# Kernel optimization log

Measured on AMD Instinct MI355X. Metric: run time of the kernel, lower is better.

Reference implementation:

```python
import jax, jax.numpy as jnp
import numpy as np

D_MODEL = 2048
NUM_HEADS = 16
HEAD_DIM = D_MODEL // NUM_HEADS
EPS = 1e-6


def setup_inputs() -> dict:
    key = jax.random.key(0)
    ks = jax.random.split(key, 5)
    B, S = 1, 4096
    scale = 1.0 / np.sqrt(D_MODEL)
    return {
        "x": jax.random.normal(ks[0], (B, S, D_MODEL), dtype=jnp.float32),
        "wq": jax.random.normal(ks[1], (D_MODEL, D_MODEL), dtype=jnp.float32) * scale,
        "wk": jax.random.normal(ks[2], (D_MODEL, D_MODEL), dtype=jnp.float32) * scale,
        "wv": jax.random.normal(ks[3], (D_MODEL, D_MODEL), dtype=jnp.float32) * scale,
        "wo": jax.random.normal(ks[4], (D_MODEL, D_MODEL), dtype=jnp.float32) * scale,
        "q_norm_w": jnp.ones((HEAD_DIM,), dtype=jnp.float32),
        "k_norm_w": jnp.ones((HEAD_DIM,), dtype=jnp.float32),
    }


def _rmsnorm(x, w):
    rms = jnp.sqrt(jnp.mean(x * x, axis=-1, keepdims=True) + EPS)
    return x / rms * w


def reference(x, wq, wk, wv, wo, q_norm_w, k_norm_w):
    B, S, _ = x.shape
    # nn.Linear: y = x @ W.T ; split heads -> [B, H, S, Dh]
    def proj(w):
        return (x @ w.T).reshape(B, S, NUM_HEADS, HEAD_DIM).transpose(0, 2, 1, 3)
    q = _rmsnorm(proj(wq), q_norm_w)
    k = _rmsnorm(proj(wk), k_norm_w)
    v = proj(wv)
    scale = 1.0 / np.sqrt(HEAD_DIM)
    attn = jnp.einsum("bhqd,bhkd->bhqk", q, k) * scale  # [B,H,S,S]
    attn = jax.nn.softmax(attn, axis=-1)
    out = jnp.einsum("bhqk,bhkd->bhqd", attn, v)
    out = out.transpose(0, 2, 1, 3).reshape(B, S, D_MODEL)
    return out @ wo.T
```

## Files before the change

kernel.cpp:

```cpp
#include <hip/hip_runtime.h>
#include <hip/hip_bf16.h>

#define S 4096
#define D 2048
#define NH 16
#define HD 128

typedef __attribute__((ext_vector_type(8))) short bf16x8;
typedef __attribute__((ext_vector_type(4))) float f32x4;

typedef __attribute__((address_space(1))) char glob_char;
typedef __attribute__((address_space(3))) char lds_char_t;

__device__ __forceinline__ void gld16(const void* g, void* l) {
    __builtin_amdgcn_global_load_lds((const glob_char*)g, (lds_char_t*)l, 16, 0, 0);
}

__device__ __forceinline__ unsigned short f2b(float f) {
    union { float f; unsigned u; } c; c.f = f;
    unsigned r = c.u + 0x7fff + ((c.u >> 16) & 1);
    return (unsigned short)(r >> 16);
}

__device__ __forceinline__ float fexp2(float x) {
#if __has_builtin(__builtin_amdgcn_exp2f)
    return __builtin_amdgcn_exp2f(x);
#else
    return __expf(x * 0.6931471805599453f);
#endif
}

__global__ __launch_bounds__(256) void cvt_all(
    const float* __restrict__ x,  const float* __restrict__ wq,
    const float* __restrict__ wk, const float* __restrict__ wv,
    const float* __restrict__ wo,
    unsigned short* __restrict__ xb, unsigned short* __restrict__ wqkvb,
    unsigned short* __restrict__ wob)
{
    const int z = blockIdx.y;
    const float* src; unsigned short* dst; int n4;
    if (z == 0)      { src = x;  dst = xb;                        n4 = (S * D) / 4; }
    else if (z == 1) { src = wq; dst = wqkvb;                     n4 = (D * D) / 4; }
    else if (z == 2) { src = wk; dst = wqkvb + (size_t)D * D;     n4 = (D * D) / 4; }
    else if (z == 3) { src = wv; dst = wqkvb + 2 * (size_t)D * D; n4 = (D * D) / 4; }
    else             { src = wo; dst = wob;                       n4 = (D * D) / 4; }
    int i = blockIdx.x * 256 + threadIdx.x;
    if (i < n4) {
        float4 v = ((const float4*)src)[i];
        ushort4 o;
        o.x = f2b(v.x); o.y = f2b(v.y); o.z = f2b(v.z); o.w = f2b(v.w);
        ((ushort4*)dst)[i] = o;
    }
}

template<int OUTMODE>
__global__ __launch_bounds__(256) void gemm_nt(
    const unsigned short* __restrict__ A, const unsigned short* __restrict__ B,
    void* __restrict__ O0, void* __restrict__ O1, void* __restrict__ O2,
    const float* __restrict__ qw, const float* __restrict__ kw)
{
    __shared__ short As[128 * 32];
    __shared__ short Bs[128 * 32];
    __shared__ float red[2][128];

    const int tid = threadIdx.x;
    const int m0 = blockIdx.y * 128, n0 = blockIdx.x * 128;
    const int w = tid >> 6, lane = tid & 63, col = lane & 15, quad = lane >> 4;
    const int mw = (w >> 1) * 64, nw = (w & 1) * 64;

    const int r0 = tid >> 2, k80 = (tid & 3) << 3;
    const size_t aoff = (size_t)(m0 + r0) * 2048 + k80;
    const size_t boff = (size_t)(n0 + r0) * 2048 + k80;

    f32x4 acc[4][4];
    #pragma unroll
    for (int i = 0; i < 4; ++i)
        #pragma unroll
        for (int j = 0; j < 4; ++j)
            #pragma unroll
            for (int r = 0; r < 4; ++r) acc[i][j][r] = 0.0f;

    for (int k0 = 0; k0 < 2048; k0 += 32) {
        gld16(&A[aoff + k0],               &As[tid * 8]);
        gld16(&A[aoff + 64 * 2048 + k0],   &As[(tid + 256) * 8]);
        gld16(&B[boff + k0],               &Bs[tid * 8]);
        gld16(&B[boff + 64 * 2048 + k0],   &Bs[(tid + 256) * 8]);
        __syncthreads();
        bf16x8 af[4], bf[4];
        #pragma unroll
        for (int i = 0; i < 4; ++i)
            af[i] = *(const bf16x8*)&As[(mw + 16 * i + col) * 32 + quad * 8];
        #pragma unroll
        for (int j = 0; j < 4; ++j)
            bf[j] = *(const bf16x8*)&Bs[(nw + 16 * j + col) * 32 + quad * 8];
        #pragma unroll
        for (int i = 0; i < 4; ++i)
            #pragma unroll
            for (int j = 0; j < 4; ++j)
                acc[i][j] = __builtin_amdgcn_mfma_f32_16x16x32_bf16(af[i], bf[j], acc[i][j], 0, 0, 0);
        __syncthreads();
    }

    if (OUTMODE == 1) {
        float* C = (float*)O0;
        #pragma unroll
        for (int i = 0; i < 4; ++i)
            #pragma unroll
            for (int j = 0; j < 4; ++j)
                #pragma unroll
                for (int r = 0; r < 4; ++r)
                    C[(size_t)(m0 + mw + 16 * i + quad * 4 + r) * 2048 + n0 + nw + 16 * j + col] = acc[i][j][r];
    } else {
        const int sel = n0 >> 11;
        if (sel == 2) {
            unsigned short* VtO = (unsigned short*)O2;
            #pragma unroll
            for (int i = 0; i < 4; ++i)
                #pragma unroll
                for (int j = 0; j < 4; ++j) {
                    int n = (n0 & 2047) + nw + 16 * j + col;
                    int hh = n >> 7, dv = n & 127;
                    ushort4 pk;
                    pk.x = f2b(acc[i][j][0]); pk.y = f2b(acc[i][j][1]);
                    pk.z = f2b(acc[i][j][2]); pk.w = f2b(acc[i][j][3]);
                    *(ushort4*)&VtO[(size_t)hh * (HD * S) + (size_t)dv * S +
                                    m0 + mw + 16 * i + quad * 4] = pk;
                }
        } else {
            unsigned short* C = (unsigned short*)(sel == 0 ? O0 : O1);
            const int nc0 = (n0 & 2047) + nw + col;
            const float* wgt = (sel == 0) ? qw : kw;
            const float extra = (sel == 0)
                ? 0.08838834764831845f * 1.4426950408889634f : 1.0f;
            float wv[4];
            #pragma unroll
            for (int j = 0; j < 4; ++j) wv[j] = wgt[nw + 16 * j + col];
            float rsc[4][4];
            #pragma unroll
            for (int i = 0; i < 4; ++i)
                #pragma unroll
                for (int r = 0; r < 4; ++r) {
                    float ss = 0.0f;
                    #pragma unroll
                    for (int j = 0; j < 4; ++j) ss += acc[i][j][r] * acc[i][j][r];
                    #pragma unroll
                    for (int d = 1; d < 16; d <<= 1) ss += __shfl_xor(ss, d, 64);
                    if (col == 0) red[w & 1][mw + 16 * i + quad * 4 + r] = ss;
                }
            __syncthreads();
            #pragma unroll
            for (int i = 0; i < 4; ++i)
                #pragma unroll
                for (int r = 0; r < 4; ++r) {
                    float tot = red[0][mw + 16 * i + quad * 4 + r] + red[1][mw + 16 * i + quad * 4 + r];
                    rsc[i][r] = rsqrtf(tot * (1.0f / HD) + 1e-6f) * extra;
                }
            #pragma unroll
            for (int i = 0; i < 4; ++i)
                #pragma unroll
                for (int j = 0; j < 4; ++j)
                    #pragma unroll
                    for (int r = 0; r < 4; ++r)
                        C[(size_t)(m0 + mw + 16 * i + quad * 4 + r) * 2048 + nc0 + 16 * j] =
                            f2b(acc[i][j][r] * rsc[i][r] * wv[j]);
        }
    }
}

struct FlashSmem {
    short Ks[2][8192];
    short Vs[2][8192];
    short Ps[8192];
};

__global__ __launch_bounds__(256, 2) void flash_mfma(
    const unsigned short* __restrict__ Qg, const unsigned short* __restrict__ Kg,
    const unsigned short* __restrict__ Vt, unsigned short* __restrict__ Ctx)
{
    __shared__ FlashSmem sm;

    const int tid = threadIdx.x;
    const int w = tid >> 6, lane = tid & 63, col = lane & 15, quad = lane >> 4;
    const int q0 = blockIdx.x * 128, h = blockIdx.y;

    bf16x8 aq[2][4];
    #pragma unroll
    for (int qs = 0; qs < 2; ++qs) {
        const size_t qoff = (size_t)(q0 + w * 32 + qs * 16 + col) * 2048 + h * 128 + quad * 8;
        #pragma unroll
        for (int ds = 0; ds < 4; ++ds)
            aq[qs][ds] = *(const bf16x8*)&Qg[qoff + ds * 32];
    }

    const unsigned short* kga[4];
    const unsigned short* vga[4];
    #pragma unroll
    for (int it = 0; it < 4; ++it) {
        int c = tid + (it << 8);
        {   int ds = c >> 8, rem = c & 255, key = rem >> 2, ch = rem & 3;
            int g = ch ^ ((key >> 1) & 3);
            kga[it] = &Kg[(size_t)key * 2048 + h * 128 + ds * 32 + g * 8]; }
        {   int ks = c >> 9, rem = c & 511, dv = rem >> 2, ch = rem & 3;
            int g = ch ^ ((dv >> 1) & 3);
            vga[it] = &Vt[(size_t)h * (HD * S) + (size_t)dv * S + ks * 32 + g * 8]; }
    }

    const int fb = col * 32 + ((quad ^ ((col >> 1) & 3)) << 3);
    int ap_off[2][2];
    #pragma unroll
    for (int qs = 0; qs < 2; ++qs) {
        int qrow = w * 32 + qs * 16 + col;
        #pragma unroll
        for (int ks = 0; ks < 2; ++ks) {
            int k0 = ks * 32 + quad * 8;
            ap_off[ks][qs] = qrow * 64 + (k0 ^ ((qrow & 7) << 3));
        }
    }
    int psb2[2][4];
    #pragma unroll
    for (int qs = 0; qs < 2; ++qs)
        #pragma unroll
        for (int r = 0; r < 4; ++r) {
            int ql = w * 32 + qs * 16 + quad * 4 + r;
            int s = (ql & 7) << 3;
            psb2[qs][r] = ql * 64 + (col ^ (s & 8)) + (s & 48);
        }

    bf16x8 vone;
    #pragma unroll
    for (int i = 0; i < 8; ++i) vone[i] = (short)0x3F80;

    f32x4 lacc[2];
    f32x4 o[2][8];
    #pragma unroll
    for (int qs = 0; qs < 2; ++qs) {
        #pragma unroll
        for (int r = 0; r < 4; ++r) lacc[qs][r] = 0.0f;
        #pragma unroll
        for (int nj = 0; nj < 8; ++nj)
            #pragma unroll
            for (int r = 0; r < 4; ++r) o[qs][nj][r] = 0.0f;
    }

    auto stage = [&](int b) {
        #pragma unroll
        for (int it = 0; it < 4; ++it) {
            gld16(kga[it], &sm.Ks[b][(tid + (it << 8)) * 8]);
            kga[it] += 64 * 2048;
        }
        #pragma unroll
        for (int it = 0; it < 4; ++it) {
            gld16(vga[it], &sm.Vs[b][(tid + (it << 8)) * 8]);
            vga[it] += 64;
        }
    };

    auto compute = [&](int b) {
        f32x4 sc[2][4];
        #pragma unroll
        for (int qs = 0; qs < 2; ++qs)
            #pragma unroll
            for (int kj = 0; kj < 4; ++kj)
                #pragma unroll
                for (int r = 0; r < 4; ++r) sc[qs][kj][r] = 0.0f;
        __builtin_amdgcn_s_setprio(1);
        #pragma unroll
        for (int ds = 0; ds < 4; ++ds)
            #pragma unroll
            for (int kj = 0; kj < 4; ++kj) {
                bf16x8 bk = *(const bf16x8*)&sm.Ks[b][fb + ds * 2048 + kj * 512];
                sc[0][kj] = __builtin_amdgcn_mfma_f32_16x16x32_bf16(aq[0][ds], bk, sc[0][kj], 0, 0, 0);
                sc[1][kj] = __builtin_amdgcn_mfma_f32_16x16x32_bf16(aq[1][ds], bk, sc[1][kj], 0, 0, 0);
            }
        __builtin_amdgcn_s_setprio(0);

        #pragma unroll
        for (int qs = 0; qs < 2; ++qs)
            #pragma unroll
            for (int kj = 0; kj < 4; ++kj)
                #pragma unroll
                for (int r = 0; r < 4; ++r)
                    sm.Ps[psb2[qs][r] ^ (kj * 16)] = (short)f2b(fexp2(sc[qs][kj][r]));

        __builtin_amdgcn_s_setprio(1);
        #pragma unroll
        for (int ks = 0; ks < 2; ++ks) {
            bf16x8 ap0 = *(const bf16x8*)&sm.Ps[ap_off[ks][0]];
            bf16x8 ap1 = *(const bf16x8*)&sm.Ps[ap_off[ks][1]];
            lacc[0] = __builtin_amdgcn_mfma_f32_16x16x32_bf16(ap0, vone, lacc[0], 0, 0, 0);
            lacc[1] = __builtin_amdgcn_mfma_f32_16x16x32_bf16(ap1, vone, lacc[1], 0, 0, 0);
            #pragma unroll
            for (int nj = 0; nj < 8; ++nj) {
                bf16x8 bv = *(const bf16x8*)&sm.Vs[b][fb + ks * 4096 + nj * 512];
                o[0][nj] = __builtin_amdgcn_mfma_f32_16x16x32_bf16(ap0, bv, o[0][nj], 0, 0, 0);
                o[1][nj] = __builtin_amdgcn_mfma_f32_16x16x32_bf16(ap1, bv, o[1][nj], 0, 0, 0);
            }
        }
        __builtin_amdgcn_s_setprio(0);
    };

    stage(0);
    for (int j0 = 0; j0 < S; j0 += 128) {
        __syncthreads();
        stage(1);
        compute(0);
        __syncthreads();
        if (j0 + 128 < S) stage(0);
        compute(1);
    }

    #pragma unroll
    for (int qs = 0; qs < 2; ++qs) {
        float inv[4];
        #pragma unroll
        for (int r = 0; r < 4; ++r) inv[r] = 1.0f / lacc[qs][r];
        #pragma unroll
        for (int nj = 0; nj < 8; ++nj)
            #pragma unroll
            for (int r = 0; r < 4; ++r)
                Ctx[(size_t)(q0 + w * 32 + qs * 16 + quad * 4 + r) * 2048 + h * 128 + nj * 16 + col] =
                    f2b(o[qs][nj][r] * inv[r]);
    }
}

extern "C" void kernel_launch(void* const* d_in, const int* in_sizes, int n_in,
                              void* d_out, int out_size, void* d_ws, size_t ws_size,
                              hipStream_t stream)
{
    const float* x  = (const float*)d_in[0];
    const float* wq = (const float*)d_in[1];
    const float* wk = (const float*)d_in[2];
    const float* wv = (const float*)d_in[3];
    const float* wo = (const float*)d_in[4];
    const float* qw = (const float*)d_in[5];
    const float* kw = (const float*)d_in[6];
    float* out = (float*)d_out;

    const size_t MB = 1u << 20;
    char* ws = (char*)d_ws;
    unsigned short* xb    = (unsigned short*)(ws);
    unsigned short* Wqkvb = (unsigned short*)(ws + 16 * MB);
    unsigned short* Wob   = (unsigned short*)(ws + 40 * MB);
    unsigned short* Qb    = (unsigned short*)(ws + 48 * MB);
    unsigned short* Kb    = (unsigned short*)(ws + 64 * MB);
    unsigned short* Vt    = (unsigned short*)(ws + 80 * MB);
    unsigned short* Ctx   = xb;

    cvt_all<<<dim3(8192, 5), dim3(256), 0, stream>>>(x, wq, wk, wv, wo, xb, Wqkvb, Wob);

    gemm_nt<0><<<dim3(48, 32), dim3(256), 0, stream>>>(xb, Wqkvb, Qb, Kb, Vt, qw, kw);

    flash_mfma<<<dim3(32, 16), dim3(256), 0, stream>>>(Qb, Kb, Vt, Ctx);

    gemm_nt<1><<<dim3(16, 32), dim3(256), 0, stream>>>(Ctx, Wob, out, out, out, qw, kw);
}
```

Baseline: 472.5 us.

## Replace GEMM with 256x256-tile 8-wave kernel using swizzled double-buffered LDS pipeline

Replaces the 128x128 single-buffered GEMM with a 256x256 tile, 512-thread kernel that uses a 64-wide K step, XOR-swizzled LDS layout and double-buffered asynchronous global-to-LDS loads interleaved with four MFMA phases per iteration. The aim is more reuse per loaded byte, fewer LDS bank conflicts, and global load latency hidden behind MFMA work instead of a full sync per k-step. The RMSNorm epilogue is adapted to the new wave layout. The costs are higher register pressure (128 accumulators per lane), a 128KB LDS footprint, and fewer blocks (128 for the output projection), which may underfill the GPU.

```diff
diff --git a/kernel.cpp b/kernel.cpp
--- a/kernel.cpp
+++ b/kernel.cpp
@@ -29,6 +29,8 @@
     return __expf(x * 0.6931471805599453f);
 #endif
 }
+
+#define MFMA16(a, b, c) __builtin_amdgcn_mfma_f32_16x16x32_bf16((a), (b), (c), 0, 0, 0)
 
 __global__ __launch_bounds__(256) void cvt_all(
     const float* __restrict__ x,  const float* __restrict__ wq,
@@ -54,115 +56,193 @@
 }
 
 template<int OUTMODE>
-__global__ __launch_bounds__(256) void gemm_nt(
+__global__ __launch_bounds__(512, 2) void gemm8(
     const unsigned short* __restrict__ A, const unsigned short* __restrict__ B,
     void* __restrict__ O0, void* __restrict__ O1, void* __restrict__ O2,
     const float* __restrict__ qw, const float* __restrict__ kw)
 {
-    __shared__ short As[128 * 32];
-    __shared__ short Bs[128 * 32];
-    __shared__ float red[2][128];
+    __shared__ short lds[65536];
+    __shared__ float red[4][256];
 
     const int tid = threadIdx.x;
-    const int m0 = blockIdx.y * 128, n0 = blockIdx.x * 128;
-    const int w = tid >> 6, lane = tid & 63, col = lane & 15, quad = lane >> 4;
-    const int mw = (w >> 1) * 64, nw = (w & 1) * 64;
-
-    const int r0 = tid >> 2, k80 = (tid & 3) << 3;
-    const size_t aoff = (size_t)(m0 + r0) * 2048 + k80;
-    const size_t boff = (size_t)(n0 + r0) * 2048 + k80;
-
-    f32x4 acc[4][4];
-    #pragma unroll
-    for (int i = 0; i < 4; ++i)
+    const int lane = tid & 63, col = lane & 15, quad = lane >> 4;
+    const int w = tid >> 6, wr = w >> 2, wc = w & 3;
+    const int m0 = blockIdx.y * 256, n0 = blockIdx.x * 256;
+
+    const int srow = tid >> 3;
+    const int sslot = (tid & 7) ^ (srow & 7);
+    const unsigned short* pa0 = A + (size_t)(m0 + srow) * 2048 + sslot * 8;
+    const unsigned short* pb0 = B + (size_t)(n0 + srow) * 2048 + sslot * 8;
+    const int dst0 = tid * 8;
+
+    auto stA = [&](int t, int h, int buf) {
+        const unsigned short* g = pa0 + (size_t)h * 262144 + t * 64;
+        short* d = &lds[buf * 16384 + h * 8192 + dst0];
+        gld16(g, d);
+        gld16(g + 131072, d + 4096);
+    };
+    auto stB = [&](int t, int h, int buf) {
+        const unsigned short* g = pb0 + (size_t)h * 262144 + t * 64;
+        short* d = &lds[32768 + buf * 16384 + h * 8192 + dst0];
+        gld16(g, d);
+        gld16(g + 131072, d + 4096);
+    };
+
+    const int sl0 = (quad ^ (col & 7)) << 3;
+    const int arow = (wr * 128 + col) * 64;
+    const int brow = (wc * 64 + col) * 64;
+    auto rdA = [&](int mf, int kk, int buf) -> bf16x8 {
+        return *(const bf16x8*)&lds[buf * 16384 + arow + mf * 1024 + (sl0 ^ (kk << 5))];
+    };
+    auto rdB = [&](int nf, int kk, int buf) -> bf16x8 {
+        return *(const bf16x8*)&lds[32768 + buf * 16384 + brow + nf * 1024 + (sl0 ^ (kk << 5))];
+    };
+
+    f32x4 acc[8][4];
+    #pragma unroll
+    for (int i = 0; i < 8; ++i)
         #pragma unroll
         for (int j = 0; j < 4; ++j)
             #pragma unroll
             for (int r = 0; r < 4; ++r) acc[i][j][r] = 0.0f;
 
-    for (int k0 = 0; k0 < 2048; k0 += 32) {
-        gld16(&A[aoff + k0],               &As[tid * 8]);
-        gld16(&A[aoff + 64 * 2048 + k0],   &As[(tid + 256) * 8]);
-        gld16(&B[boff + k0],               &Bs[tid * 8]);
-        gld16(&B[boff + 64 * 2048 + k0],   &Bs[(tid + 256) * 8]);
-        __syncthreads();
-        bf16x8 af[4], bf[4];
-        #pragma unroll
-        for (int i = 0; i < 4; ++i)
-            af[i] = *(const bf16x8*)&As[(mw + 16 * i + col) * 32 + quad * 8];
-        #pragma unroll
-        for (int j = 0; j < 4; ++j)
-            bf[j] = *(const bf16x8*)&Bs[(nw + 16 * j + col) * 32 + quad * 8];
-        #pragma unroll
-        for (int i = 0; i < 4; ++i)
-            #pragma unroll
-            for (int j = 0; j < 4; ++j)
-                acc[i][j] = __builtin_amdgcn_mfma_f32_16x16x32_bf16(af[i], bf[j], acc[i][j], 0, 0, 0);
-        __syncthreads();
+    stA(0, 0, 0); stA(0, 1, 0); stB(0, 0, 0); stB(0, 1, 0);
+    stA(1, 0, 1); stA(1, 1, 1);
+    asm volatile("s_waitcnt vmcnt(4)" ::: "memory");
+    __builtin_amdgcn_s_barrier();
+
+    for (int t = 0; t < 32; ++t) {
+        const int cur = t & 1, nxt = cur ^ 1;
+        const bool s1 = t < 31, s2 = t < 30;
+        bf16x8 a0[4][2], a1[4][2], b0[2][2], b1[2][2];
+
+        #pragma unroll
+        for (int mf = 0; mf < 4; ++mf) { a0[mf][0] = rdA(mf, 0, cur); a0[mf][1] = rdA(mf, 1, cur); }
+        #pragma unroll
+        for (int nf = 0; nf < 2; ++nf) { b0[nf][0] = rdB(nf, 0, cur); b0[nf][1] = rdB(nf, 1, cur); }
+        if (s1) stB(t + 1, 0, nxt);
+        __builtin_amdgcn_s_barrier();
+        __builtin_amdgcn_s_setprio(1);
+        #pragma unroll
+        for (int mf = 0; mf < 4; ++mf)
+            #pragma unroll
+            for (int nf = 0; nf < 2; ++nf) {
+                acc[mf][nf] = MFMA16(a0[mf][0], b0[nf][0], acc[mf][nf]);
+                acc[mf][nf] = MFMA16(a0[mf][1], b0[nf][1], acc[mf][nf]);
+            }
+        __builtin_amdgcn_s_setprio(0);
+        __builtin_amdgcn_s_barrier();
+
+        #pragma unroll
+        for (int mf = 0; mf < 4; ++mf) { a1[mf][0] = rdA(mf + 4, 0, cur); a1[mf][1] = rdA(mf + 4, 1, cur); }
+        #pragma unroll
+        for (int nf = 0; nf < 2; ++nf) { b1[nf][0] = rdB(nf + 2, 0, cur); b1[nf][1] = rdB(nf + 2, 1, cur); }
+        if (s1) stB(t + 1, 1, nxt);
+        __builtin_amdgcn_s_barrier();
+        __builtin_amdgcn_s_setprio(1);
+        #pragma unroll
+        for (int mf = 0; mf < 4; ++mf)
+            #pragma unroll
+            for (int nf = 0; nf < 2; ++nf) {
+                acc[mf][nf + 2] = MFMA16(a0[mf][0], b1[nf][0], acc[mf][nf + 2]);
+                acc[mf][nf + 2] = MFMA16(a0[mf][1], b1[nf][1], acc[mf][nf + 2]);
+            }
+        __builtin_amdgcn_s_setprio(0);
+        __builtin_amdgcn_s_barrier();
+
+        if (s2) stA(t + 2, 0, cur);
+        __builtin_amdgcn_s_barrier();
+        __builtin_amdgcn_s_setprio(1);
+        #pragma unroll
+        for (int mf = 0; mf < 4; ++mf)
+            #pragma unroll
+            for (int nf = 0; nf < 2; ++nf) {
+                acc[mf + 4][nf] = MFMA16(a1[mf][0], b0[nf][0], acc[mf + 4][nf]);
+                acc[mf + 4][nf] = MFMA16(a1[mf][1], b0[nf][1], acc[mf + 4][nf]);
+            }
+        __builtin_amdgcn_s_setprio(0);
+        __builtin_amdgcn_s_barrier();
+
+        if (s2) stA(t + 2, 1, cur);
+        __builtin_amdgcn_s_barrier();
+        __builtin_amdgcn_s_setprio(1);
+        #pragma unroll
+        for (int mf = 0; mf < 4; ++mf)
+            #pragma unroll
+            for (int nf = 0; nf < 2; ++nf) {
+                acc[mf + 4][nf + 2] = MFMA16(a1[mf][0], b1[nf][0], acc[mf + 4][nf + 2]);
+                acc[mf + 4][nf + 2] = MFMA16(a1[mf][1], b1[nf][1], acc[mf + 4][nf + 2]);
+            }
+        __builtin_amdgcn_s_setprio(0);
+        if (s2)      asm volatile("s_waitcnt vmcnt(4)" ::: "memory");
+        else if (s1) asm volatile("s_waitcnt vmcnt(0)" ::: "memory");
+        __builtin_amdgcn_s_barrier();
     }
 
     if (OUTMODE == 1) {
         float* C = (float*)O0;
         #pragma unroll
-        for (int i = 0; i < 4; ++i)
-            #pragma unroll
-            for (int j = 0; j < 4; ++j)
+        for (int mf = 0; mf < 8; ++mf)
+            #pragma unroll
+            for (int nf = 0; nf < 4; ++nf)
                 #pragma unroll
                 for (int r = 0; r < 4; ++r)
-                    C[(size_t)(m0 + mw + 16 * i + quad * 4 + r) * 2048 + n0 + nw + 16 * j + col] = acc[i][j][r];
+                    C[(size_t)(m0 + wr * 128 + mf * 16 + quad * 4 + r) * 2048 +
+                      n0 + wc * 64 + nf * 16 + col] = acc[mf][nf][r];
     } else {
         const int sel = n0 >> 11;
         if (sel == 2) {
             unsigned short* VtO = (unsigned short*)O2;
             #pragma unroll
-            for (int i = 0; i < 4; ++i)
-                #pragma unroll
-                for (int j = 0; j < 4; ++j) {
-                    int n = (n0 & 2047) + nw + 16 * j + col;
+            for (int mf = 0; mf < 8; ++mf)
+                #pragma unroll
+                for (int nf = 0; nf < 4; ++nf) {
+                    int n = (n0 & 2047) + wc * 64 + nf * 16 + col;
                     int hh = n >> 7, dv = n & 127;
                     ushort4 pk;
-                    pk.x = f2b(acc[i][j][0]); pk.y = f2b(acc[i][j][1]);
-                    pk.z = f2b(acc[i][j][2]); pk.w = f2b(acc[i][j][3]);
+                    pk.x = f2b(acc[mf][nf][0]); pk.y = f2b(acc[mf][nf][1]);
+                    pk.z = f2b(acc[mf][nf][2]); pk.w = f2b(acc[mf][nf][3]);
                     *(ushort4*)&VtO[(size_t)hh * (HD * S) + (size_t)dv * S +
-                                    m0 + mw + 16 * i + quad * 4] = pk;
+                                    m0 + wr * 128 + mf * 16 + quad * 4] = pk;
                 }
         } else {
             unsigned short* C = (unsigned short*)(sel == 0 ? O0 : O1);
-            const int nc0 = (n0 & 2047) + nw + col;
             const float* wgt = (sel == 0) ? qw : kw;
             const float extra = (sel == 0)
                 ? 0.08838834764831845f * 1.4426950408889634f : 1.0f;
-            float wv[4];
-            #pragma unroll
-            for (int j = 0; j < 4; ++j) wv[j] = wgt[nw + 16 * j + col];
-            float rsc[4][4];
-            #pragma unroll
-            for (int i = 0; i < 4; ++i)
+            float wv4[4];
+            #pragma unroll
+            for (int nf = 0; nf < 4; ++nf)
+                wv4[nf] = wgt[(wc & 1) * 64 + nf * 16 + col];
+            #pragma unroll
+            for (int mf = 0; mf < 8; ++mf)
                 #pragma unroll
                 for (int r = 0; r < 4; ++r) {
                     float ss = 0.0f;
                     #pragma unroll
-                    for (int j = 0; j < 4; ++j) ss += acc[i][j][r] * acc[i][j][r];
+                    for (int nf = 0; nf < 4; ++nf) ss += acc[mf][nf][r] * acc[mf][nf][r];
                     #pragma unroll
                     for (int d = 1; d < 16; d <<= 1) ss += __shfl_xor(ss, d, 64);
-                    if (col == 0) red[w & 1][mw + 16 * i + quad * 4 + r] = ss;
+                    if (col == 0) red[wc][wr * 128 + mf * 16 + quad * 4 + r] = ss;
                 }
             __syncthreads();
             #pragma unroll
-            for (int i = 0; i < 4; ++i)
+            for (int mf = 0; mf < 8; ++mf) {
+                float rsc[4];
                 #pragma unroll
                 for (int r = 0; r < 4; ++r) {
-                    float tot = red[0][mw + 16 * i + quad * 4 + r] + red[1][mw + 16 * i + quad * 4 + r];
-                    rsc[i][r] = rsqrtf(tot * (1.0f / HD) + 1e-6f) * extra;
+                    int idx = wr * 128 + mf * 16 + quad * 4 + r;
+                    float tot = red[wc & 6][idx] + red[(wc & 6) + 1][idx];
+                    rsc[r] = rsqrtf(tot * (1.0f / HD) + 1e-6f) * extra;
                 }
-            #pragma unroll
-            for (int i = 0; i < 4; ++i)
-                #pragma unroll
-                for (int j = 0; j < 4; ++j)
+                #pragma unroll
+                for (int nf = 0; nf < 4; ++nf)
                     #pragma unroll
                     for (int r = 0; r < 4; ++r)
-                        C[(size_t)(m0 + mw + 16 * i + quad * 4 + r) * 2048 + nc0 + 16 * j] =
-                            f2b(acc[i][j][r] * rsc[i][r] * wv[j]);
+                        C[(size_t)(m0 + wr * 128 + mf * 16 + quad * 4 + r) * 2048 +
+                          (n0 & 2047) + wc * 64 + nf * 16 + col] =
+                            f2b(acc[mf][nf][r] * rsc[r] * wv4[nf]);
+            }
         }
     }
 }
@@ -269,8 +349,8 @@
             #pragma unroll
             for (int kj = 0; kj < 4; ++kj) {
                 bf16x8 bk = *(const bf16x8*)&sm.Ks[b][fb + ds * 2048 + kj * 512];
-                sc[0][kj] = __builtin_amdgcn_mfma_f32_16x16x32_bf16(aq[0][ds], bk, sc[0][kj], 0, 0, 0);
-                sc[1][kj] = __builtin_amdgcn_mfma_f32_16x16x32_bf16(aq[1][ds], bk, sc[1][kj], 0, 0, 0);
+                sc[0][kj] = MFMA16(aq[0][ds], bk, sc[0][kj]);
+                sc[1][kj] = MFMA16(aq[1][ds], bk, sc[1][kj]);
             }
         __builtin_amdgcn_s_setprio(0);
 
@@ -287,13 +367,13 @@
         for (int ks = 0; ks < 2; ++ks) {
             bf16x8 ap0 = *(const bf16x8*)&sm.Ps[ap_off[ks][0]];
             bf16x8 ap1 = *(const bf16x8*)&sm.Ps[ap_off[ks][1]];
-            lacc[0] = __builtin_amdgcn_mfma_f32_16x16x32_bf16(ap0, vone, lacc[0], 0, 0, 0);
-            lacc[1] = __builtin_amdgcn_mfma_f32_16x16x32_bf16(ap1, vone, lacc[1], 0, 0, 0);
+            lacc[0] = MFMA16(ap0, vone, lacc[0]);
+            lacc[1] = MFMA16(ap1, vone, lacc[1]);
             #pragma unroll
             for (int nj = 0; nj < 8; ++nj) {
                 bf16x8 bv = *(const bf16x8*)&sm.Vs[b][fb + ks * 4096 + nj * 512];
-                o[0][nj] = __builtin_amdgcn_mfma_f32_16x16x32_bf16(ap0, bv, o[0][nj], 0, 0, 0);
-                o[1][nj] = __builtin_amdgcn_mfma_f32_16x16x32_bf16(ap1, bv, o[1][nj], 0, 0, 0);
+                o[0][nj] = MFMA16(ap0, bv, o[0][nj]);
+                o[1][nj] = MFMA16(ap1, bv, o[1][nj]);
             }
         }
         __builtin_amdgcn_s_setprio(0);
@@ -348,9 +428,9 @@
 
     cvt_all<<<dim3(8192, 5), dim3(256), 0, stream>>>(x, wq, wk, wv, wo, xb, Wqkvb, Wob);
 
-    gemm_nt<0><<<dim3(48, 32), dim3(256), 0, stream>>>(xb, Wqkvb, Qb, Kb, Vt, qw, kw);
+    gemm8<0><<<dim3(24, 16), dim3(512), 0, stream>>>(xb, Wqkvb, Qb, Kb, Vt, qw, kw);
 
     flash_mfma<<<dim3(32, 16), dim3(256), 0, stream>>>(Qb, Kb, Vt, Ctx);
 
-    gemm_nt<1><<<dim3(16, 32), dim3(256), 0, stream>>>(Ctx, Wob, out, out, out, qw, kw);
-}
+    gemm8<1><<<dim3(8, 16), dim3(512), 0, stream>>>(Ctx, Wob, out, out, out, qw, kw);
+}
```

New measurement: 454.5 us. 3.8% less time.
